# Kernel optimization log

Hardware: AMD Instinct MI355X
Metric: run time of the kernel (lower is better)

## Reference

```python
import jax, jax.numpy as jnp
import numpy as np

N_NODES = 100000
N_EDGES = 1600000
DIM = 128
N_LAYERS = 3


def setup_inputs() -> dict:
    key = jax.random.key(0)
    k1, k2, k3, k4 = jax.random.split(key, 4)
    inputs = jax.random.normal(k1, (N_NODES, DIM), dtype=jnp.float32)
    Ws = jax.random.normal(k2, (N_LAYERS, DIM, DIM), dtype=jnp.float32) * (DIM ** -0.5)
    bs = jnp.zeros((N_LAYERS, DIM), dtype=jnp.float32)
    src = jax.random.randint(k3, (N_EDGES,), 0, N_NODES, dtype=jnp.int32)
    dst = jax.random.randint(k4, (N_EDGES,), 0, N_NODES, dtype=jnp.int32)
    return {"inputs": inputs, "Ws": Ws, "bs": bs, "src": src, "dst": dst}


def reference(inputs, Ws, bs, src, dst):
    N = inputs.shape[0]
    L = Ws.shape[0]
    # dgl.add_self_loop: append one self-edge per node
    loop = jnp.arange(N, dtype=src.dtype)
    src_f = jnp.concatenate([src, loop])
    dst_f = jnp.concatenate([dst, loop])
    ones = jnp.ones(src_f.shape[0], dtype=inputs.dtype)
    deg_out = jax.ops.segment_sum(ones, src_f, num_segments=N)  # out-degree
    deg_in = jax.ops.segment_sum(ones, dst_f, num_segments=N)   # in-degree
    # norm='both': symmetric normalization; self-loops guarantee deg >= 1
    norm_src = jax.lax.rsqrt(deg_out)[:, None]
    norm_dst = jax.lax.rsqrt(deg_in)[:, None]
    h = inputs
    for l in range(L):
        hs = h * norm_src                               # [N, d]
        m = jax.ops.segment_sum(hs[src_f], dst_f, num_segments=N)  # aggregate
        m = m * norm_dst
        h = m @ Ws[l] + bs[l]
        if l < L - 1:
            h = jax.nn.relu(h)
    return h
```

## Files before the change

### kernel.cpp

```cpp
#include <hip/hip_runtime.h>
#include <hip/hip_fp16.h>
#include <cstddef>

#define NN 100000
#define NE 1600000
#define DIM 128
#define WND 196
#define WSH 9
#define WSZ 512
#define CAP 8960
#define NSTR 96
#define EPB 2048
#define LSTR 136

typedef _Float16 half8 __attribute__((ext_vector_type(8)));
typedef float floatx4 __attribute__((ext_vector_type(4)));

__global__ __launch_bounds__(256) void phase1(
    const int* __restrict__ src, const int* __restrict__ dst,
    int* __restrict__ gcurd, int* __restrict__ gcurs,
    unsigned* __restrict__ dstbuk, unsigned short* __restrict__ srcbuk) {
  __shared__ int cntd[WND], cnts[WND], based[WND], bases[WND];
  const int tid = threadIdx.x;
  const int e0 = blockIdx.x * EPB + tid;
  for (int i = tid; i < WND; i += 256) { cntd[i] = 0; cnts[i] = 0; }
  __syncthreads();
  int ss[8], dd[8]; bool val[8];
  #pragma unroll
  for (int u = 0; u < 8; ++u) {
    int e = e0 + u * 256;
    val[u] = e < NE;
    ss[u] = val[u] ? src[e] : 0;
    dd[u] = val[u] ? dst[e] : 0;
    if (val[u]) {
      atomicAdd(&cntd[dd[u] >> WSH], 1);
      atomicAdd(&cnts[ss[u] >> WSH], 1);
    }
  }
  __syncthreads();
  for (int i = tid; i < WND; i += 256) {
    based[i] = atomicAdd(&gcurd[i], cntd[i]);
    bases[i] = atomicAdd(&gcurs[i], cnts[i]);
    cntd[i] = 0; cnts[i] = 0;
  }
  __syncthreads();
  #pragma unroll
  for (int u = 0; u < 8; ++u) {
    if (!val[u]) continue;
    int wd = dd[u] >> WSH;
    int p = based[wd] + atomicAdd(&cntd[wd], 1);
    if (p < CAP)
      dstbuk[(size_t)wd * CAP + p] =
          ((unsigned)(dd[u] & (WSZ - 1)) << 17) | (unsigned)ss[u];
    int ws = ss[u] >> WSH;
    int q = bases[ws] + atomicAdd(&cnts[ws], 1);
    if (q < CAP)
      srcbuk[(size_t)ws * CAP + q] = (unsigned short)(ss[u] & (WSZ - 1));
  }
}

__global__ __launch_bounds__(512) void phase2d(
    const unsigned* __restrict__ dstbuk, const int* __restrict__ gcurd,
    int* __restrict__ col, int* __restrict__ fillt, float* __restrict__ ndst) {
  __shared__ int cur[WSZ];
  const int w = blockIdx.x, tid = threadIdx.x;
  const int n = min(gcurd[w], CAP);
  for (int i = tid; i < WSZ; i += 512) cur[i] = 0;
  __syncthreads();
  const size_t base = (size_t)w * CAP;
  for (int i = tid; i < n; i += 512) {
    unsigned u = dstbuk[base + i];
    int s = u & 0x1FFFF;
    int dl = u >> 17;
    int p = atomicAdd(&cur[dl], 1);
    if (p < NSTR) col[(size_t)((w << WSH) + dl) * NSTR + p] = s;
  }
  __syncthreads();
  for (int i = tid; i < WSZ; i += 512) {
    int v = (w << WSH) + i;
    if (v < NN) {
      int d = cur[i];
      fillt[v] = d < NSTR ? d : NSTR;
      ndst[v] = rsqrtf((float)(d + 1));
    }
  }
}

__global__ __launch_bounds__(512) void phase2s(
    const unsigned short* __restrict__ srcbuk, const int* __restrict__ gcurs,
    float* __restrict__ nsrc) {
  __shared__ int cnt[WSZ];
  const int w = blockIdx.x, tid = threadIdx.x;
  const int n = min(gcurs[w], CAP);
  for (int i = tid; i < WSZ; i += 512) cnt[i] = 0;
  __syncthreads();
  const size_t base = (size_t)w * CAP;
  for (int i = tid; i < n; i += 512)
    atomicAdd(&cnt[srcbuk[base + i]], 1);
  __syncthreads();
  for (int i = tid; i < WSZ; i += 512) {
    int v = (w << WSH) + i;
    if (v < NN) nsrc[v] = rsqrtf((float)(cnt[i] + 1));
  }
}

__global__ __launch_bounds__(256) void wprep(
    const float* __restrict__ W, __half* __restrict__ Wt) {
  int idx = blockIdx.x * 256 + threadIdx.x;
  if (idx >= 3 * DIM * DIM) return;
  int l = idx / (DIM * DIM);
  int r = idx - l * DIM * DIM;
  int k = r >> 7, n = r & 127;
  Wt[(size_t)l * DIM * DIM + n * DIM + k] = __float2half(W[idx]);
}

__global__ __launch_bounds__(256) void scale_kernel(
    const float* __restrict__ x, const float* __restrict__ nsrc,
    __half* __restrict__ hs) {
  int idx = blockIdx.x * 256 + threadIdx.x;
  if (idx >= NN * (DIM / 8)) return;
  int row = idx >> 4;
  float ns = nsrc[row];
  float4 a = ((const float4*)x)[idx * 2];
  float4 b = ((const float4*)x)[idx * 2 + 1];
  __half2 h[4];
  h[0] = __floats2half2_rn(a.x * ns, a.y * ns);
  h[1] = __floats2half2_rn(a.z * ns, a.w * ns);
  h[2] = __floats2half2_rn(b.x * ns, b.y * ns);
  h[3] = __floats2half2_rn(b.z * ns, b.w * ns);
  *(uint4*)(hs + (size_t)idx * 8) = *(uint4*)h;
}

__global__ __launch_bounds__(256) void agg_kernel(
    const __half* __restrict__ hs, const int* __restrict__ col,
    const int* __restrict__ fillt, const float* __restrict__ ndst,
    __half* __restrict__ m) {
  const int wid  = (blockIdx.x * 256 + threadIdx.x) >> 6;
  const int lane = threadIdx.x & 63;
  const int v = 4 * wid + (lane >> 4);
  if (v >= NN) return;
  const int f  = lane & 15;
  const int fi = f * 8;
  const int qb = lane & 48;
  const size_t base = (size_t)v * NSTR;

  const int   cnt = fillt[v];
  const float nd  = ndst[v];
  int c0 = col[base + f];
  int c1 = col[base + 16 + f];
  uint4 qself = *(const uint4*)(hs + (size_t)v * DIM + fi);

  int mx = cnt;
  { int o = __shfl_xor(mx, 16); mx = o > mx ? o : mx; }
  { int o = __shfl_xor(mx, 32); mx = o > mx ? o : mx; }

  float acc[8];
  {
    const __half2* hp = (const __half2*)&qself;
    #pragma unroll
    for (int j = 0; j < 4; ++j) {
      float2 t = __half22float2(hp[j]);
      acc[2 * j] = t.x; acc[2 * j + 1] = t.y;
    }
  }

  #define BATCH16(creg, tbase)                                              \
  {                                                                         \
    unsigned off[16]; float msk[16];                                        \
    _Pragma("unroll")                                                       \
    for (int u = 0; u < 16; ++u) {                                          \
      int s = __shfl((creg), qb + u);                                       \
      bool valid = ((tbase) + u) < cnt;                                     \
      off[u] = (unsigned)(valid ? s : v) * DIM + fi;                        \
      msk[u] = valid ? 1.f : 0.f;                                           \
    }                                                                       \
    uint4 q[16];                                                            \
    _Pragma("unroll")                                                       \
    for (int u = 0; u < 16; ++u) q[u] = *(const uint4*)(hs + off[u]);       \
    _Pragma("unroll")                                                       \
    for (int u = 0; u < 16; ++u) {                                          \
      const __half2* hp2 = (const __half2*)&q[u];                           \
      _Pragma("unroll")                                                     \
      for (int j = 0; j < 4; ++j) {                                         \
        float2 t2 = __half22float2(hp2[j]);                                 \
        acc[2 * j]     = fmaf(t2.x, msk[u], acc[2 * j]);                    \
        acc[2 * j + 1] = fmaf(t2.y, msk[u], acc[2 * j + 1]);                \
      }                                                                     \
    }                                                                       \
  }

  BATCH16(c0, 0);
  if (mx > 16) {
    BATCH16(c1, 16);
    if (mx > 32) {
      for (int tb = 32; tb < mx; tb += 8) {
        int ss[8]; float msk[8];
        #pragma unroll
        for (int u = 0; u < 8; ++u) {
          int t = tb + u;
          bool valid = t < cnt;
          int ci = valid ? t : 0;
          int s = col[base + ci];
          ss[u]  = valid ? s : v;
          msk[u] = valid ? 1.f : 0.f;
        }
        #pragma unroll
        for (int u = 0; u < 8; ++u) {
          uint4 q = *(const uint4*)(hs + (size_t)ss[u] * DIM + fi);
          const __half2* hp2 = (const __half2*)&q;
          #pragma unroll
          for (int j = 0; j < 4; ++j) {
            float2 t2 = __half22float2(hp2[j]);
            acc[2 * j]     = fmaf(t2.x, msk[u], acc[2 * j]);
            acc[2 * j + 1] = fmaf(t2.y, msk[u], acc[2 * j + 1]);
          }
        }
      }
    }
  }
  #undef BATCH16

  __half2 hh[4];
  #pragma unroll
  for (int j = 0; j < 4; ++j)
    hh[j] = __floats2half2_rn(acc[2 * j] * nd, acc[2 * j + 1] * nd);
  *(uint4*)(m + (size_t)v * DIM + fi) = *(uint4*)hh;
}

__global__ __launch_bounds__(256, 2) void gemm_mfma(
    const __half* __restrict__ m, const __half* __restrict__ Wt,
    const float* __restrict__ b, const float* __restrict__ nsrc,
    __half* __restrict__ hsb, float* __restrict__ out, int last) {
  __shared__ _Float16 sM[DIM * LSTR];
  __shared__ _Float16 sWt[DIM * LSTR];
  const int tid  = threadIdx.x;
  const int wv   = tid >> 6;
  const int lane = tid & 63;
  const int l15  = lane & 15;
  const int quad = lane >> 4;
  const int row0 = blockIdx.x * DIM;

  #pragma unroll
  for (int t = 0; t < 8; ++t) {
    int idx = tid + t * 256;
    int r = idx >> 4, c8 = idx & 15;
    int gr = row0 + r; gr = gr < NN ? gr : NN - 1;
    uint4 vm = *(const uint4*)(m + (size_t)gr * DIM + c8 * 8);
    *(uint4*)&sM[r * LSTR + c8 * 8] = vm;
    uint4 vw = *(const uint4*)(Wt + (size_t)r * DIM + c8 * 8);
    *(uint4*)&sWt[r * LSTR + c8 * 8] = vw;
  }
  __syncthreads();

  floatx4 acc[2][8] = {};
  #pragma unroll
  for (int kc = 0; kc < 4; ++kc) {
    const int ko = kc * 32 + quad * 8;
    half8 a0 = *(const half8*)&sM[(wv * 32 + l15) * LSTR + ko];
    half8 a1 = *(const half8*)&sM[(wv * 32 + 16 + l15) * LSTR + ko];
    #pragma unroll
    for (int cb = 0; cb < 8; ++cb) {
      half8 bf = *(const half8*)&sWt[(cb * 16 + l15) * LSTR + ko];
      acc[0][cb] = __builtin_amdgcn_mfma_f32_16x16x32_f16(a0, bf, acc[0][cb], 0, 0, 0);
      acc[1][cb] = __builtin_amdgcn_mfma_f32_16x16x32_f16(a1, bf, acc[1][cb], 0, 0, 0);
    }
  }

  #pragma unroll
  for (int rb = 0; rb < 2; ++rb) {
    #pragma unroll
    for (int r = 0; r < 4; ++r) {
      int grow = row0 + wv * 32 + rb * 16 + quad * 4 + r;
      if (grow >= NN) continue;
      float ns = last ? 0.f : nsrc[grow];
      #pragma unroll
      for (int cb = 0; cb < 8; ++cb) {
        int gcol = cb * 16 + l15;
        float o = acc[rb][cb][r] + b[gcol];
        if (!last) {
          o = fmaxf(o, 0.f) * ns;
          hsb[(size_t)grow * DIM + gcol] = __float2half(o);
        } else {
          out[(size_t)grow * DIM + gcol] = o;
        }
      }
    }
  }
}

extern "C" void kernel_launch(void* const* d_in, const int* in_sizes, int n_in,
                              void* d_out, int out_size, void* d_ws, size_t ws_size,
                              hipStream_t stream) {
  const float* inputs = (const float*)d_in[0];
  const float* Ws     = (const float*)d_in[1];
  const float* bs     = (const float*)d_in[2];
  const int*   src    = (const int*)d_in[3];
  const int*   dst    = (const int*)d_in[4];
  float* out = (float*)d_out;
  int* col = (int*)d_out;

  __half*         mbuf   = (__half*)d_ws;
  unsigned*       dstbuk = (unsigned*)d_ws;
  unsigned short* srcbuk = (unsigned short*)(dstbuk + (size_t)WND * CAP);
  __half*         hsbuf  = mbuf + (size_t)NN * DIM;
  __half*         Wt     = hsbuf + (size_t)NN * DIM;
  int*            gcurd  = (int*)(Wt + 3 * DIM * DIM);
  int*            gcurs  = gcurd + WND;
  int*            fillt  = gcurs + WND;
  float*          nsrc   = (float*)(fillt + NN);
  float*          ndst   = nsrc + NN;

  hipMemsetAsync(gcurd, 0, 2 * WND * sizeof(int), stream);
  phase1<<<(NE + EPB - 1) / EPB, 256, 0, stream>>>(src, dst, gcurd, gcurs,
                                                   dstbuk, srcbuk);
  phase2d<<<WND, 512, 0, stream>>>(dstbuk, gcurd, col, fillt, ndst);
  phase2s<<<WND, 512, 0, stream>>>(srcbuk, gcurs, nsrc);
  wprep<<<(3 * DIM * DIM + 255) / 256, 256, 0, stream>>>(Ws, Wt);
  scale_kernel<<<(NN * (DIM / 8) + 255) / 256, 256, 0, stream>>>(inputs, nsrc, hsbuf);

  for (int l = 0; l < 3; ++l) {
    agg_kernel<<<(NN / 4 + 3) / 4, 256, 0, stream>>>(hsbuf, col, fillt, ndst, mbuf);
    gemm_mfma<<<(NN + DIM - 1) / DIM, 256, 0, stream>>>(
        mbuf, Wt + (size_t)l * DIM * DIM, bs + (size_t)l * DIM, nsrc,
        hsbuf, out, l == 2);
  }
}
```

Baseline: 444.4 us.

## Fuse neighbor aggregation into the MFMA GEMM for the first two layers

After: 388.7 us. 12.5% less time.

```diff
diff --git a/kernel.cpp b/kernel.cpp
--- a/kernel.cpp
+++ b/kernel.cpp
@@ -131,6 +131,72 @@
   *(uint4*)(hs + (size_t)idx * 8) = *(uint4*)h;
 }
 
+__device__ __forceinline__ void agg_core(
+    const __half* __restrict__ hs, const int* __restrict__ col,
+    size_t base, int v, int cnt, int qb, int f, int fi, float* acc) {
+  int c0 = col[base + f];
+  int c1 = col[base + 16 + f];
+  uint4 qself = *(const uint4*)(hs + (size_t)v * DIM + fi);
+
+  int mx = cnt;
+  { int o = __shfl_xor(mx, 16); mx = o > mx ? o : mx; }
+  { int o = __shfl_xor(mx, 32); mx = o > mx ? o : mx; }
+
+  const float coef = (float)((cnt < 32 ? cnt : 32) - 31);
+  {
+    const __half2* hp = (const __half2*)&qself;
+    #pragma unroll
+    for (int j = 0; j < 4; ++j) {
+      float2 t = __half22float2(hp[j]);
+      acc[2 * j] = coef * t.x; acc[2 * j + 1] = coef * t.y;
+    }
+  }
+
+  uint4 q[32];
+  #pragma unroll
+  for (int u = 0; u < 32; ++u) {
+    int s = (u < 16) ? __shfl(c0, qb + u) : __shfl(c1, qb + (u - 16));
+    unsigned off = (unsigned)(u < cnt ? s : v) * DIM + fi;
+    q[u] = *(const uint4*)(hs + off);
+  }
+  __builtin_amdgcn_sched_barrier(0);
+  #pragma unroll
+  for (int u = 0; u < 32; ++u) {
+    const __half2* hp2 = (const __half2*)&q[u];
+    #pragma unroll
+    for (int j = 0; j < 4; ++j) {
+      float2 t2 = __half22float2(hp2[j]);
+      acc[2 * j]     += t2.x;
+      acc[2 * j + 1] += t2.y;
+    }
+  }
+
+  if (mx > 32) {
+    for (int tb = 32; tb < mx; tb += 8) {
+      int ss[8]; float msk[8];
+      #pragma unroll
+      for (int u = 0; u < 8; ++u) {
+        int t = tb + u;
+        bool valid = t < cnt;
+        int s = col[base + (valid ? t : 0)];
+        ss[u]  = valid ? s : v;
+        msk[u] = valid ? 1.f : 0.f;
+      }
+      #pragma unroll
+      for (int u = 0; u < 8; ++u) {
+        uint4 qq = *(const uint4*)(hs + (size_t)ss[u] * DIM + fi);
+        const __half2* hp2 = (const __half2*)&qq;
+        #pragma unroll
+        for (int j = 0; j < 4; ++j) {
+          float2 t2 = __half22float2(hp2[j]);
+          acc[2 * j]     = fmaf(t2.x, msk[u], acc[2 * j]);
+          acc[2 * j + 1] = fmaf(t2.y, msk[u], acc[2 * j + 1]);
+        }
+      }
+    }
+  }
+}
+
 __global__ __launch_bounds__(256) void agg_kernel(
     const __half* __restrict__ hs, const int* __restrict__ col,
     const int* __restrict__ fillt, const float* __restrict__ ndst,
@@ -138,87 +204,15 @@
   const int wid  = (blockIdx.x * 256 + threadIdx.x) >> 6;
   const int lane = threadIdx.x & 63;
   const int v = 4 * wid + (lane >> 4);
-  if (v >= NN) return;
   const int f  = lane & 15;
   const int fi = f * 8;
   const int qb = lane & 48;
   const size_t base = (size_t)v * NSTR;
-
-  const int   cnt = fillt[v];
-  const float nd  = ndst[v];
-  int c0 = col[base + f];
-  int c1 = col[base + 16 + f];
-  uint4 qself = *(const uint4*)(hs + (size_t)v * DIM + fi);
-
-  int mx = cnt;
-  { int o = __shfl_xor(mx, 16); mx = o > mx ? o : mx; }
-  { int o = __shfl_xor(mx, 32); mx = o > mx ? o : mx; }
+  const int cnt = fillt[v];
+  const float nd = ndst[v];
 
   float acc[8];
-  {
-    const __half2* hp = (const __half2*)&qself;
-    #pragma unroll
-    for (int j = 0; j < 4; ++j) {
-      float2 t = __half22float2(hp[j]);
-      acc[2 * j] = t.x; acc[2 * j + 1] = t.y;
-    }
-  }
-
-  #define BATCH16(creg, tbase)                                              \
-  {                                                                         \
-    unsigned off[16]; float msk[16];                                        \
-    _Pragma("unroll")                                                       \
-    for (int u = 0; u < 16; ++u) {                                          \
-      int s = __shfl((creg), qb + u);                                       \
-      bool valid = ((tbase) + u) < cnt;                                     \
-      off[u] = (unsigned)(valid ? s : v) * DIM + fi;                        \
-      msk[u] = valid ? 1.f : 0.f;                                           \
-    }                                                                       \
-    uint4 q[16];                                                            \
-    _Pragma("unroll")                                                       \
-    for (int u = 0; u < 16; ++u) q[u] = *(const uint4*)(hs + off[u]);       \
-    _Pragma("unroll")                                                       \
-    for (int u = 0; u < 16; ++u) {                                          \
-      const __half2* hp2 = (const __half2*)&q[u];                           \
-      _Pragma("unroll")                                                     \
-      for (int j = 0; j < 4; ++j) {                                         \
-        float2 t2 = __half22float2(hp2[j]);                                 \
-        acc[2 * j]     = fmaf(t2.x, msk[u], acc[2 * j]);                    \
-        acc[2 * j + 1] = fmaf(t2.y, msk[u], acc[2 * j + 1]);                \
-      }                                                                     \
-    }                                                                       \
-  }
-
-  BATCH16(c0, 0);
-  if (mx > 16) {
-    BATCH16(c1, 16);
-    if (mx > 32) {
-      for (int tb = 32; tb < mx; tb += 8) {
-        int ss[8]; float msk[8];
-        #pragma unroll
-        for (int u = 0; u < 8; ++u) {
-          int t = tb + u;
-          bool valid = t < cnt;
-          int ci = valid ? t : 0;
-          int s = col[base + ci];
-          ss[u]  = valid ? s : v;
-          msk[u] = valid ? 1.f : 0.f;
-        }
-        #pragma unroll
-        for (int u = 0; u < 8; ++u) {
-          uint4 q = *(const uint4*)(hs + (size_t)ss[u] * DIM + fi);
-          const __half2* hp2 = (const __half2*)&q;
-          #pragma unroll
-          for (int j = 0; j < 4; ++j) {
-            float2 t2 = __half22float2(hp2[j]);
-            acc[2 * j]     = fmaf(t2.x, msk[u], acc[2 * j]);
-            acc[2 * j + 1] = fmaf(t2.y, msk[u], acc[2 * j + 1]);
-          }
-        }
-      }
-    }
-  }
-  #undef BATCH16
+  agg_core(hs, col, base, v, cnt, qb, f, fi, acc);
 
   __half2 hh[4];
   #pragma unroll
@@ -227,10 +221,85 @@
   *(uint4*)(m + (size_t)v * DIM + fi) = *(uint4*)hh;
 }
 
+__global__ __launch_bounds__(256, 2) void agg_gemm(
+    const __half* __restrict__ hs, const int* __restrict__ col,
+    const int* __restrict__ fillt, const float* __restrict__ ndst,
+    const __half* __restrict__ Wt, const float* __restrict__ b,
+    const float* __restrict__ nsrc, __half* __restrict__ hsn) {
+  __shared__ _Float16 sM[DIM * LSTR];
+  __shared__ _Float16 sWt[DIM * LSTR];
+  const int tid  = threadIdx.x;
+  const int wv   = tid >> 6;
+  const int lane = tid & 63;
+  const int l15  = lane & 15;
+  const int quad = lane >> 4;
+  const int f    = lane & 15;
+  const int fi   = f * 8;
+  const int qb   = lane & 48;
+  const int row0 = blockIdx.x * DIM;
+
+  #pragma unroll
+  for (int t = 0; t < 8; ++t) {
+    int idx = tid + t * 256;
+    int r = idx >> 4, c8 = idx & 15;
+    uint4 vw = *(const uint4*)(Wt + (size_t)r * DIM + c8 * 8);
+    *(uint4*)&sWt[r * LSTR + c8 * 8] = vw;
+  }
+
+  for (int p = 0; p < 8; ++p) {
+    const int r = p * 16 + wv * 4 + (lane >> 4);
+    const int v = row0 + r;
+    const int vv = v < NN ? v : NN - 1;
+    const size_t base = (size_t)vv * NSTR;
+    const int cnt = v < NN ? fillt[vv] : 0;
+    const float nd = ndst[vv];
+
+    float acc[8];
+    agg_core(hs, col, base, vv, cnt, qb, f, fi, acc);
+
+    __half2 hh[4];
+    #pragma unroll
+    for (int j = 0; j < 4; ++j)
+      hh[j] = __floats2half2_rn(acc[2 * j] * nd, acc[2 * j + 1] * nd);
+    *(uint4*)&sM[r * LSTR + fi] = *(uint4*)hh;
+  }
+  __syncthreads();
+
+  floatx4 acc[2][8] = {};
+  #pragma unroll
+  for (int kc = 0; kc < 4; ++kc) {
+    const int ko = kc * 32 + quad * 8;
+    half8 a0 = *(const half8*)&sM[(wv * 32 + l15) * LSTR + ko];
+    half8 a1 = *(const half8*)&sM[(wv * 32 + 16 + l15) * LSTR + ko];
+    #pragma unroll
+    for (int cb = 0; cb < 8; ++cb) {
+      half8 bf = *(const half8*)&sWt[(cb * 16 + l15) * LSTR + ko];
+      acc[0][cb] = __builtin_amdgcn_mfma_f32_16x16x32_f16(a0, bf, acc[0][cb], 0, 0, 0);
+      acc[1][cb] = __builtin_amdgcn_mfma_f32_16x16x32_f16(a1, bf, acc[1][cb], 0, 0, 0);
+    }
+  }
+
+  #pragma unroll
+  for (int rb = 0; rb < 2; ++rb) {
+    #pragma unroll
+    for (int r = 0; r < 4; ++r) {
+      int grow = row0 + wv * 32 + rb * 16 + quad * 4 + r;
+      if (grow >= NN) continue;
+      float ns = nsrc[grow];
+      #pragma unroll
+      for (int cb = 0; cb < 8; ++cb) {
+        int gcol = cb * 16 + l15;
+        float o = acc[rb][cb][r] + b[gcol];
+        o = fmaxf(o, 0.f) * ns;
+        hsn[(size_t)grow * DIM + gcol] = __float2half(o);
+      }
+    }
+  }
+}
+
 __global__ __launch_bounds__(256, 2) void gemm_mfma(
     const __half* __restrict__ m, const __half* __restrict__ Wt,
-    const float* __restrict__ b, const float* __restrict__ nsrc,
-    __half* __restrict__ hsb, float* __restrict__ out, int last) {
+    const float* __restrict__ b, float* __restrict__ out) {
   __shared__ _Float16 sM[DIM * LSTR];
   __shared__ _Float16 sWt[DIM * LSTR];
   const int tid  = threadIdx.x;
@@ -272,17 +341,10 @@
     for (int r = 0; r < 4; ++r) {
       int grow = row0 + wv * 32 + rb * 16 + quad * 4 + r;
       if (grow >= NN) continue;
-      float ns = last ? 0.f : nsrc[grow];
       #pragma unroll
       for (int cb = 0; cb < 8; ++cb) {
         int gcol = cb * 16 + l15;
-        float o = acc[rb][cb][r] + b[gcol];
-        if (!last) {
-          o = fmaxf(o, 0.f) * ns;
-          hsb[(size_t)grow * DIM + gcol] = __float2half(o);
-        } else {
-          out[(size_t)grow * DIM + gcol] = o;
-        }
+        out[(size_t)grow * DIM + gcol] = acc[rb][cb][r] + b[gcol];
       }
     }
   }
@@ -299,11 +361,11 @@
   float* out = (float*)d_out;
   int* col = (int*)d_out;
 
-  __half*         mbuf   = (__half*)d_ws;
+  __half*         hsA    = (__half*)d_ws;
   unsigned*       dstbuk = (unsigned*)d_ws;
   unsigned short* srcbuk = (unsigned short*)(dstbuk + (size_t)WND * CAP);
-  __half*         hsbuf  = mbuf + (size_t)NN * DIM;
-  __half*         Wt     = hsbuf + (size_t)NN * DIM;
+  __half*         hsB    = hsA + (size_t)NN * DIM;
+  __half*         Wt     = hsB + (size_t)NN * DIM;
   int*            gcurd  = (int*)(Wt + 3 * DIM * DIM);
   int*            gcurs  = gcurd + WND;
   int*            fillt  = gcurs + WND;
@@ -316,12 +378,14 @@
   phase2d<<<WND, 512, 0, stream>>>(dstbuk, gcurd, col, fillt, ndst);
   phase2s<<<WND, 512, 0, stream>>>(srcbuk, gcurs, nsrc);
   wprep<<<(3 * DIM * DIM + 255) / 256, 256, 0, stream>>>(Ws, Wt);
-  scale_kernel<<<(NN * (DIM / 8) + 255) / 256, 256, 0, stream>>>(inputs, nsrc, hsbuf);
-
-  for (int l = 0; l < 3; ++l) {
-    agg_kernel<<<(NN / 4 + 3) / 4, 256, 0, stream>>>(hsbuf, col, fillt, ndst, mbuf);
-    gemm_mfma<<<(NN + DIM - 1) / DIM, 256, 0, stream>>>(
-        mbuf, Wt + (size_t)l * DIM * DIM, bs + (size_t)l * DIM, nsrc,
-        hsbuf, out, l == 2);
-  }
-}
+  scale_kernel<<<(NN * (DIM / 8) + 255) / 256, 256, 0, stream>>>(inputs, nsrc, hsB);
+
+  const int gblk = (NN + DIM - 1) / DIM;
+  agg_gemm<<<gblk, 256, 0, stream>>>(hsB, col, fillt, ndst,
+                                     Wt, bs, nsrc, hsA);
+  agg_gemm<<<gblk, 256, 0, stream>>>(hsA, col, fillt, ndst,
+                                     Wt + (size_t)DIM * DIM, bs + DIM, nsrc, hsB);
+  agg_kernel<<<(NN / 4 + 3) / 4, 256, 0, stream>>>(hsB, col, fillt, ndst, hsA);
+  gemm_mfma<<<gblk, 256, 0, stream>>>(hsA, Wt + (size_t)2 * DIM * DIM,
+                                      bs + 2 * DIM, out);
+}
```
